# Optimization experiments

Hardware: AMD Instinct MI355X
Metric: run time of the kernel (lower is better)

## Reference

```python
import jax, jax.numpy as jnp
import numpy as np

MARGIN = 0.1
PD_EPS = 1e-6  # torch.nn.PairwiseDistance default eps (added to the difference)

B = 4096
D = 512


def setup_inputs() -> dict:
    key = jax.random.key(0)
    k1, k2, k3 = jax.random.split(key, 3)
    return {
        "feature_ts": jax.random.normal(k1, (B, D), dtype=jnp.float32),
        "feature_image1": jax.random.normal(k2, (B, D), dtype=jnp.float32),
        "feature_image2": jax.random.normal(k3, (B, D), dtype=jnp.float32),
    }


def _safe_sqrt(sq):
    # sqrt with zero gradient at 0 (matches torch.cdist backward at zero distance)
    pos = sq > 0
    return jnp.where(pos, jnp.sqrt(jnp.where(pos, sq, 1.0)), 0.0)


def reference(feature_ts, feature_image1, feature_image2):
    b, d = feature_ts.shape
    # representations: [3B, D]
    reps = jnp.concatenate([feature_ts, feature_image1, feature_image2], axis=0)

    # cdist(feature_ts, reps, p=2) -> [B, 3B] via Gram-matrix expansion
    sq = (
        jnp.sum(feature_ts * feature_ts, axis=1)[:, None]
        + jnp.sum(reps * reps, axis=1)[None, :]
        - 2.0 * (feature_ts @ reps.T)
    )
    dist = _safe_sqrt(jnp.maximum(sq, 0.0))          # [B, 3B]
    dist = jax.nn.relu(dist)                          # faithful (no-op: dist >= 0)

    # PairwiseDistance(p=2): ||x1 - x2 + eps||_2
    diff = feature_image1 - feature_image2 + PD_EPS
    dist12 = jnp.sqrt(jnp.sum(diff * diff, axis=1))   # [B]

    idx = jnp.arange(b)
    l_pos_1 = dist[idx, idx + b]                      # diag offset B
    l_pos_2 = dist[idx, idx + 2 * b]                  # diag offset 2B

    positives = l_pos_1 + l_pos_2 + dist12            # [B]
    positive_value = jnp.maximum(l_pos_1, l_pos_2)    # [B]

    # negatives: all columns except {i, i+B, i+2B}; masked min instead of gather
    cols = jnp.arange(3 * b)[None, :]
    rows = idx[:, None]
    same = (cols == rows) | (cols == rows + b) | (cols == rows + 2 * b)
    negative_value = jnp.min(jnp.where(same, jnp.inf, dist), axis=1)  # [B]

    triplet = jax.nn.relu(positives - negative_value + MARGIN) + positive_value
    return jnp.sum(triplet) / b
```

## Files before the change

### kernel.cpp

```cpp
#include <hip/hip_runtime.h>
#include <hip/hip_bf16.h>

typedef unsigned short u16;
typedef unsigned int u32;
typedef __attribute__((ext_vector_type(8))) short bf16x8;
typedef __attribute__((ext_vector_type(4))) float f32x4;

#define NB 4096
#define ND 512
#define NREPS (3*NB)
#define BM 128
#define BN 128
#define BK 64

#define GLD16(gp, lp)                                                         \
  __builtin_amdgcn_global_load_lds(                                           \
      (const __attribute__((address_space(1))) void*)(gp),                    \
      (__attribute__((address_space(3))) void*)(lp), 16, 0, 0)

__device__ __forceinline__ u16 f2bf(float f) {
  union { float f; u32 u; } v; v.f = f;
  u32 u = v.u;
  u32 r = (u + 0x7FFFu + ((u >> 16) & 1u)) >> 16;
  return (u16)r;
}

__global__ __launch_bounds__(256) void prep_all(
    const float* __restrict__ ts, const float* __restrict__ i1,
    const float* __restrict__ i2, u16* __restrict__ reps,
    float* __restrict__ norms, float* __restrict__ dist12,
    u32* __restrict__ minsq)
{
  __shared__ float s1[ND], s2[ND];
  const int r = blockIdx.x;
  const int tid = threadIdx.x;
  const int wave = tid >> 6, lane = tid & 63;

  if (wave < 3) {
    const float* src = (wave == 0) ? ts + (size_t)r * ND
                     : (wave == 1) ? i1 + (size_t)r * ND
                     :               i2 + (size_t)r * ND;
    const float4* s4 = (const float4*)src;
    float4 a = s4[lane*2+0];
    float4 b = s4[lane*2+1];
    if (wave == 1) { ((float4*)s1)[lane*2+0] = a; ((float4*)s1)[lane*2+1] = b; }
    if (wave == 2) { ((float4*)s2)[lane*2+0] = a; ((float4*)s2)[lane*2+1] = b; }
    float ss = a.x*a.x + a.y*a.y + a.z*a.z + a.w*a.w
             + b.x*b.x + b.y*b.y + b.z*b.z + b.w*b.w;
    uint4 pk;
    pk.x = (u32)f2bf(a.x) | ((u32)f2bf(a.y) << 16);
    pk.y = (u32)f2bf(a.z) | ((u32)f2bf(a.w) << 16);
    pk.z = (u32)f2bf(b.x) | ((u32)f2bf(b.y) << 16);
    pk.w = (u32)f2bf(b.z) | ((u32)f2bf(b.w) << 16);
    *(uint4*)(reps + (size_t)(wave*NB + r) * ND + lane*8) = pk;
    #pragma unroll
    for (int off = 32; off; off >>= 1) ss += __shfl_down(ss, off);
    if (lane == 0) norms[wave*NB + r] = ss;
  }
  __syncthreads();
  if (wave == 3) {
    float ss = 0.f;
    #pragma unroll
    for (int i = 0; i < 2; ++i) {
      float4 a = ((float4*)s1)[lane*2+i];
      float4 b = ((float4*)s2)[lane*2+i];
      float d0 = a.x - b.x + 1e-6f, d1 = a.y - b.y + 1e-6f;
      float d2 = a.z - b.z + 1e-6f, d3 = a.w - b.w + 1e-6f;
      ss += d0*d0 + d1*d1 + d2*d2 + d3*d3;
    }
    #pragma unroll
    for (int off = 32; off; off >>= 1) ss += __shfl_down(ss, off);
    if (lane == 0) { dist12[r] = sqrtf(ss); minsq[r] = 0x7F800000u; }
  }
}

__global__ __launch_bounds__(256) void gemm_min(
    const u16* __restrict__ reps, const float* __restrict__ norms,
    u32* __restrict__ minsq, float* __restrict__ lpos1,
    float* __restrict__ lpos2)
{
  __shared__ u16 As[BM*BK];
  __shared__ u16 Bs[BN*BK];
  const int tid  = threadIdx.x;
  const int lane = tid & 63;
  const int wave = tid >> 6;
  const int wr = wave >> 1, wc = wave & 1;
  const int fr = lane & 15, fg = lane >> 4;
  const int rowBase = blockIdx.x * BM;
  const int colBase = blockIdx.y * BN;

  const int rloc = lane >> 3;
  const int sp   = lane & 7;
  const u16* srcA[4]; const u16* srcB[4];
  u16* dstA[4]; u16* dstB[4];
  #pragma unroll
  for (int i = 0; i < 4; ++i) {
    const int r = wave*32 + i*8 + rloc;
    const int g = sp ^ (r & 7);
    srcA[i] = reps + (size_t)(rowBase + r) * ND + g*8;
    srcB[i] = reps + (size_t)(colBase + r) * ND + g*8;
    dstA[i] = &As[(wave*32 + i*8) * BK];
    dstB[i] = &Bs[(wave*32 + i*8) * BK];
  }

  f32x4 acc[4][4];
  const f32x4 zero = {0.f, 0.f, 0.f, 0.f};
  #pragma unroll
  for (int i = 0; i < 4; ++i)
    #pragma unroll
    for (int j = 0; j < 4; ++j)
      acc[i][j] = zero;

  for (int kt = 0; kt < ND/BK; ++kt) {
    const int koff = kt * BK;
    #pragma unroll
    for (int i = 0; i < 4; ++i) {
      GLD16(srcA[i] + koff, dstA[i]);
      GLD16(srcB[i] + koff, dstB[i]);
    }
    __syncthreads();

    bf16x8 af[4][2], bfrag[4][2];
    #pragma unroll
    for (int mf = 0; mf < 4; ++mf)
      #pragma unroll
      for (int ks = 0; ks < 2; ++ks) {
        const int rowA = wr*64 + mf*16 + fr;
        const int slot = ks*4 + fg;
        af[mf][ks]    = *(const bf16x8*)&As[rowA*BK + (slot ^ (rowA & 7))*8];
        const int rowB = wc*64 + mf*16 + fr;
        bfrag[mf][ks] = *(const bf16x8*)&Bs[rowB*BK + (slot ^ (rowB & 7))*8];
      }
    #pragma unroll
    for (int ks = 0; ks < 2; ++ks)
      #pragma unroll
      for (int mf = 0; mf < 4; ++mf)
        #pragma unroll
        for (int nf = 0; nf < 4; ++nf)
          acc[mf][nf] = __builtin_amdgcn_mfma_f32_16x16x32_bf16(
              af[mf][ks], bfrag[nf][ks], acc[mf][nf], 0, 0, 0);
    __syncthreads();
  }

  float ncol[4];
  #pragma unroll
  for (int nf = 0; nf < 4; ++nf)
    ncol[nf] = norms[colBase + wc*64 + nf*16 + fr];
  const float INF = __builtin_inff();
  #pragma unroll
  for (int mf = 0; mf < 4; ++mf) {
    #pragma unroll
    for (int q = 0; q < 4; ++q) {
      const int r_g = rowBase + wr*64 + mf*16 + fg*4 + q;
      const float ntr = norms[r_g];
      float vm = INF;
      #pragma unroll
      for (int nf = 0; nf < 4; ++nf) {
        const int c_g = colBase + wc*64 + nf*16 + fr;
        const float dot = acc[mf][nf][q];
        const float sq = ntr + ncol[nf] - 2.0f * dot;
        if (c_g == r_g + NB)   lpos1[r_g] = sq;
        if (c_g == r_g + 2*NB) lpos2[r_g] = sq;
        const bool excl = (c_g == r_g) || (c_g == r_g + NB) || (c_g == r_g + 2*NB);
        const float v = excl ? INF : fmaxf(sq, 0.0f);
        vm = fminf(vm, v);
      }
      #pragma unroll
      for (int off = 1; off < 16; off <<= 1)
        vm = fminf(vm, __shfl_xor(vm, off));
      if (fr == 0)
        atomicMin(minsq + r_g, __float_as_uint(vm));
    }
  }
}

__global__ __launch_bounds__(1024) void finalize(
    const float* __restrict__ lpos1, const float* __restrict__ lpos2,
    const float* __restrict__ dist12, const u32* __restrict__ minsq,
    float* __restrict__ out)
{
  __shared__ float red[16];
  const int tid = threadIdx.x;
  float s = 0.f;
  for (int r = tid; r < NB; r += 1024) {
    float l1 = sqrtf(fmaxf(lpos1[r], 0.f));
    float l2 = sqrtf(fmaxf(lpos2[r], 0.f));
    float neg = sqrtf(__uint_as_float(minsq[r]));
    float pos = l1 + l2 + dist12[r];
    s += fmaxf(pos - neg + 0.1f, 0.f) + fmaxf(l1, l2);
  }
  #pragma unroll
  for (int off = 32; off; off >>= 1) s += __shfl_down(s, off);
  if ((tid & 63) == 0) red[tid >> 6] = s;
  __syncthreads();
  if (tid == 0) {
    float t = 0.f;
    #pragma unroll
    for (int i = 0; i < 16; ++i) t += red[i];
    out[0] = t * (1.0f / NB);
  }
}

extern "C" void kernel_launch(void* const* d_in, const int* in_sizes, int n_in,
                              void* d_out, int out_size, void* d_ws, size_t ws_size,
                              hipStream_t stream) {
  const float* ts = (const float*)d_in[0];
  const float* i1 = (const float*)d_in[1];
  const float* i2 = (const float*)d_in[2];
  float* out = (float*)d_out;

  char* p = (char*)d_ws;
  u16* reps    = (u16*)p;            p += (size_t)NREPS * ND * sizeof(u16);
  float* norms = (float*)p;          p += (size_t)NREPS * sizeof(float);
  float* dist12 = (float*)p;         p += (size_t)NB * sizeof(float);
  u32* minsq   = (u32*)p;            p += (size_t)NB * sizeof(u32);
  float* lpos1 = (float*)p;          p += (size_t)NB * sizeof(float);
  float* lpos2 = (float*)p;          p += (size_t)NB * sizeof(float);

  prep_all<<<NB, 256, 0, stream>>>(ts, i1, i2, reps, norms, dist12, minsq);
  dim3 grid(NB / BM, NREPS / BN);
  gemm_min<<<grid, 256, 0, stream>>>(reps, norms, minsq, lpos1, lpos2);
  finalize<<<1, 1024, 0, stream>>>(lpos1, lpos2, dist12, minsq, out);
}
```

Before: 161.0 us.

## Use 256x256 tiles with double-buffered, quarter-staged load/MFMA pipeline

Grows the GEMM tile to 256x256 with 8 waves and double-buffers the LDS tiles. Global-to-LDS loads for the next k-step are split into quarters and interleaved with four MFMA quadrants, gated by explicit vmcnt waits, raw barriers and setprio. Workgroup IDs are remapped so neighbouring blocks share operand rows in L2. The aim is to hide load latency and raise data reuse per block, at the cost of more registers and LDS per block and a fragile hand-tuned wait schedule.

```diff
diff --git a/kernel.cpp b/kernel.cpp
--- a/kernel.cpp
+++ b/kernel.cpp
@@ -9,14 +9,18 @@
 #define NB 4096
 #define ND 512
 #define NREPS (3*NB)
-#define BM 128
-#define BN 128
+#define BM 256
+#define BN 256
 #define BK 64
+#define NKT (ND/BK)
+#define TSZ (BM*BK)
 
 #define GLD16(gp, lp)                                                         \
   __builtin_amdgcn_global_load_lds(                                           \
       (const __attribute__((address_space(1))) void*)(gp),                    \
       (__attribute__((address_space(3))) void*)(lp), 16, 0, 0)
+#define VMW asm volatile("s_waitcnt vmcnt(10)" ::: "memory")
+#define BAR __builtin_amdgcn_s_barrier()
 
 __device__ __forceinline__ u16 f2bf(float f) {
   union { float f; u32 u; } v; v.f = f;
@@ -74,72 +78,107 @@
   }
 }
 
-__global__ __launch_bounds__(256) void gemm_min(
+__device__ __forceinline__ void rdA(const u16* __restrict__ S, int wr, int fr,
+                                    int fg, int mfB, bf16x8 a[4][2]) {
+  #pragma unroll
+  for (int mf = 0; mf < 4; ++mf)
+    #pragma unroll
+    for (int ks = 0; ks < 2; ++ks) {
+      const int ra = wr*128 + (mfB+mf)*16 + fr;
+      a[mf][ks] = *(const bf16x8*)&S[ra*BK + ((ks*4+fg) ^ (ra & 7))*8];
+    }
+}
+__device__ __forceinline__ void rdB(const u16* __restrict__ S, int wc, int fr,
+                                    int fg, int nfB, bf16x8 b[2][2]) {
+  #pragma unroll
+  for (int nf = 0; nf < 2; ++nf)
+    #pragma unroll
+    for (int ks = 0; ks < 2; ++ks) {
+      const int rb = wc*64 + (nfB+nf)*16 + fr;
+      b[nf][ks] = *(const bf16x8*)&S[rb*BK + ((ks*4+fg) ^ (rb & 7))*8];
+    }
+}
+__device__ __forceinline__ void q_mfma(const bf16x8 a[4][2], const bf16x8 b[2][2],
+                                       f32x4 acc[8][4], int mfB, int nfB) {
+  #pragma unroll
+  for (int ks = 0; ks < 2; ++ks)
+    #pragma unroll
+    for (int mf = 0; mf < 4; ++mf)
+      #pragma unroll
+      for (int nf = 0; nf < 2; ++nf)
+        acc[mfB+mf][nfB+nf] = __builtin_amdgcn_mfma_f32_16x16x32_bf16(
+            a[mf][ks], b[nf][ks], acc[mfB+mf][nfB+nf], 0, 0, 0);
+}
+
+__global__ __launch_bounds__(512) void gemm_min(
     const u16* __restrict__ reps, const float* __restrict__ norms,
     u32* __restrict__ minsq, float* __restrict__ lpos1,
     float* __restrict__ lpos2)
 {
-  __shared__ u16 As[BM*BK];
-  __shared__ u16 Bs[BN*BK];
+  __shared__ u16 As[2*TSZ];
+  __shared__ u16 Bs[2*TSZ];
   const int tid  = threadIdx.x;
   const int lane = tid & 63;
   const int wave = tid >> 6;
-  const int wr = wave >> 1, wc = wave & 1;
+  const int wr = wave >> 2;
+  const int wc = wave & 3;
   const int fr = lane & 15, fg = lane >> 4;
-  const int rowBase = blockIdx.x * BM;
-  const int colBase = blockIdx.y * BN;
-
-  const int rloc = lane >> 3;
-  const int sp   = lane & 7;
-  const u16* srcA[4]; const u16* srcB[4];
-  u16* dstA[4]; u16* dstB[4];
-  #pragma unroll
-  for (int i = 0; i < 4; ++i) {
-    const int r = wave*32 + i*8 + rloc;
-    const int g = sp ^ (r & 7);
-    srcA[i] = reps + (size_t)(rowBase + r) * ND + g*8;
-    srcB[i] = reps + (size_t)(colBase + r) * ND + g*8;
-    dstA[i] = &As[(wave*32 + i*8) * BK];
-    dstB[i] = &Bs[(wave*32 + i*8) * BK];
-  }
-
-  f32x4 acc[4][4];
+
+  const int wid = (blockIdx.x & 7) * 96 + (blockIdx.x >> 3);
+  const int mx = wid & 15, ny = wid >> 4;
+  const int rowBase = mx * BM;
+  const int colBase = ny * BN;
+
+  const int c0 = wave * 2;
+  const int rA0 = (c0 < 8) ? c0*8 : 128 + (c0-8)*8;
+  const int rB0 = (c0 >> 2)*64 + (c0 & 3)*8;
+  const int gsw = (lane & 7) ^ (lane >> 3);
+  const u16* gA = reps + (size_t)(rowBase + rA0 + (lane>>3))*ND + gsw*8;
+  const u16* gB = reps + (size_t)(colBase + rB0 + (lane>>3))*ND + gsw*8;
+  u16* lA = As + rA0*BK;
+  u16* lB = Bs + rB0*BK;
+
+#define ST_ALO(b,k) { GLD16(gA + (k),         lA + (b)*TSZ);          \
+                      GLD16(gA + 8*ND + (k),  lA + (b)*TSZ + 8*BK); }
+#define ST_AHI(b,k) { GLD16(gA + 64*ND + (k), lA + (b)*TSZ + 64*BK);  \
+                      GLD16(gA + 72*ND + (k), lA + (b)*TSZ + 72*BK); }
+#define ST_BLO(b,k) { GLD16(gB + (k),         lB + (b)*TSZ);          \
+                      GLD16(gB + 8*ND + (k),  lB + (b)*TSZ + 8*BK); }
+#define ST_BHI(b,k) { GLD16(gB + 32*ND + (k), lB + (b)*TSZ + 32*BK);  \
+                      GLD16(gB + 40*ND + (k), lB + (b)*TSZ + 40*BK); }
+
+  f32x4 acc[8][4];
   const f32x4 zero = {0.f, 0.f, 0.f, 0.f};
   #pragma unroll
-  for (int i = 0; i < 4; ++i)
-    #pragma unroll
-    for (int j = 0; j < 4; ++j)
-      acc[i][j] = zero;
-
-  for (int kt = 0; kt < ND/BK; ++kt) {
-    const int koff = kt * BK;
-    #pragma unroll
-    for (int i = 0; i < 4; ++i) {
-      GLD16(srcA[i] + koff, dstA[i]);
-      GLD16(srcB[i] + koff, dstB[i]);
-    }
-    __syncthreads();
-
-    bf16x8 af[4][2], bfrag[4][2];
-    #pragma unroll
-    for (int mf = 0; mf < 4; ++mf)
-      #pragma unroll
-      for (int ks = 0; ks < 2; ++ks) {
-        const int rowA = wr*64 + mf*16 + fr;
-        const int slot = ks*4 + fg;
-        af[mf][ks]    = *(const bf16x8*)&As[rowA*BK + (slot ^ (rowA & 7))*8];
-        const int rowB = wc*64 + mf*16 + fr;
-        bfrag[mf][ks] = *(const bf16x8*)&Bs[rowB*BK + (slot ^ (rowB & 7))*8];
-      }
-    #pragma unroll
-    for (int ks = 0; ks < 2; ++ks)
-      #pragma unroll
-      for (int mf = 0; mf < 4; ++mf)
-        #pragma unroll
-        for (int nf = 0; nf < 4; ++nf)
-          acc[mf][nf] = __builtin_amdgcn_mfma_f32_16x16x32_bf16(
-              af[mf][ks], bfrag[nf][ks], acc[mf][nf], 0, 0, 0);
-    __syncthreads();
+  for (int i = 0; i < 8; ++i)
+    #pragma unroll
+    for (int j = 0; j < 4; ++j) acc[i][j] = zero;
+
+  bf16x8 aLo[4][2], aHi[4][2], bb[2][2];
+
+  ST_ALO(0, 0); ST_BLO(0, 0); ST_AHI(0, 0); ST_BHI(0, 0);
+  ST_ALO(1, BK); ST_BLO(1, BK); ST_AHI(1, BK);
+
+  for (int t = 0; t < NKT; ++t) {
+    const int cur = t & 1, nxt = cur ^ 1;
+    const u16* Sa = As + cur*TSZ;
+    const u16* Sb = Bs + cur*TSZ;
+    const int k1 = (t+1)*BK, k2 = (t+2)*BK;
+    VMW; ST_BHI(nxt, k1);
+    rdA(Sa, wr, fr, fg, 0, aLo); rdB(Sb, wc, fr, fg, 0, bb);
+    __builtin_amdgcn_s_setprio(1); q_mfma(aLo, bb, acc, 0, 0);
+    __builtin_amdgcn_s_setprio(0); BAR;
+    VMW; ST_ALO(cur, k2);
+    rdA(Sa, wr, fr, fg, 4, aHi);
+    __builtin_amdgcn_s_setprio(1); q_mfma(aHi, bb, acc, 4, 0);
+    __builtin_amdgcn_s_setprio(0); BAR;
+    VMW; ST_BLO(cur, k2);
+    rdB(Sb, wc, fr, fg, 2, bb);
+    __builtin_amdgcn_s_setprio(1); q_mfma(aLo, bb, acc, 0, 2);
+    __builtin_amdgcn_s_setprio(0); BAR;
+    VMW; ST_AHI(cur, k2);
+    __builtin_amdgcn_s_setprio(1); q_mfma(aHi, bb, acc, 4, 2);
+    __builtin_amdgcn_s_setprio(0); BAR;
   }
 
   float ncol[4];
@@ -148,10 +187,10 @@
     ncol[nf] = norms[colBase + wc*64 + nf*16 + fr];
   const float INF = __builtin_inff();
   #pragma unroll
-  for (int mf = 0; mf < 4; ++mf) {
+  for (int mf = 0; mf < 8; ++mf) {
     #pragma unroll
     for (int q = 0; q < 4; ++q) {
-      const int r_g = rowBase + wr*64 + mf*16 + fg*4 + q;
+      const int r_g = rowBase + wr*128 + mf*16 + fg*4 + q;
       const float ntr = norms[r_g];
       float vm = INF;
       #pragma unroll
@@ -218,7 +257,6 @@
   float* lpos2 = (float*)p;          p += (size_t)NB * sizeof(float);
 
   prep_all<<<NB, 256, 0, stream>>>(ts, i1, i2, reps, norms, dist12, minsq);
-  dim3 grid(NB / BM, NREPS / BN);
-  gemm_min<<<grid, 256, 0, stream>>>(reps, norms, minsq, lpos1, lpos2);
+  gemm_min<<<(NB/BM) * (NREPS/BN), 512, 0, stream>>>(reps, norms, minsq, lpos1, lpos2);
   finalize<<<1, 1024, 0, stream>>>(lpos1, lpos2, dist12, minsq, out);
 }
```

Result: slower. 189.2 us (+17.5%).

## Double-buffer LDS tiles in GEMM and remap blocks for XCD-aware locality

Applied to the files above, without the earlier changes.

Doubles the LDS A/B tiles so the global-to-LDS loads for the next K step are issued before the MFMA work on the current step, with one barrier per iteration instead of two. It also flattens the grid and remaps block IDs so consecutive blocks on each of the 8 XCDs cover nearby output tiles, aiming to improve L2 reuse. The cost is double the LDS per block (64KB), which may lower occupancy. The single barrier per iteration depends on the async LDS loads being complete by the time that barrier is reached.

```diff
diff --git a/kernel.cpp b/kernel.cpp
--- a/kernel.cpp
+++ b/kernel.cpp
@@ -12,6 +12,8 @@
 #define BM 128
 #define BN 128
 #define BK 64
+#define NKT (ND/BK)
+#define TSZ (BM*BK)
 
 #define GLD16(gp, lp)                                                         \
   __builtin_amdgcn_global_load_lds(                                           \
@@ -79,15 +81,19 @@
     u32* __restrict__ minsq, float* __restrict__ lpos1,
     float* __restrict__ lpos2)
 {
-  __shared__ u16 As[BM*BK];
-  __shared__ u16 Bs[BN*BK];
+  __shared__ u16 As[2*TSZ];
+  __shared__ u16 Bs[2*TSZ];
   const int tid  = threadIdx.x;
   const int lane = tid & 63;
   const int wave = tid >> 6;
   const int wr = wave >> 1, wc = wave & 1;
   const int fr = lane & 15, fg = lane >> 4;
-  const int rowBase = blockIdx.x * BM;
-  const int colBase = blockIdx.y * BN;
+
+  const int bid = blockIdx.x;
+  const int wid = (bid & 7) * 384 + (bid >> 3);
+  const int mx = wid / 96, ny = wid % 96;
+  const int rowBase = mx * BM;
+  const int colBase = ny * BN;
 
   const int rloc = lane >> 3;
   const int sp   = lane & 7;
@@ -103,6 +109,13 @@
     dstB[i] = &Bs[(wave*32 + i*8) * BK];
   }
 
+#define STAGE(buf, koff)                                                      \
+  { _Pragma("unroll")                                                         \
+    for (int i = 0; i < 4; ++i) {                                             \
+      GLD16(srcA[i] + (koff), dstA[i] + (buf)*TSZ);                           \
+      GLD16(srcB[i] + (koff), dstB[i] + (buf)*TSZ);                           \
+    } }
+
   f32x4 acc[4][4];
   const f32x4 zero = {0.f, 0.f, 0.f, 0.f};
   #pragma unroll
@@ -111,36 +124,39 @@
     for (int j = 0; j < 4; ++j)
       acc[i][j] = zero;
 
-  for (int kt = 0; kt < ND/BK; ++kt) {
-    const int koff = kt * BK;
-    #pragma unroll
-    for (int i = 0; i < 4; ++i) {
-      GLD16(srcA[i] + koff, dstA[i]);
-      GLD16(srcB[i] + koff, dstB[i]);
-    }
+#define COMPUTE(cur)                                                          \
+  { const u16* Sa = As + (cur)*TSZ;                                           \
+    const u16* Sb = Bs + (cur)*TSZ;                                           \
+    bf16x8 af[4][2], bfr[4][2];                                               \
+    _Pragma("unroll")                                                         \
+    for (int mf = 0; mf < 4; ++mf)                                            \
+      _Pragma("unroll")                                                       \
+      for (int ks = 0; ks < 2; ++ks) {                                        \
+        const int rowA = wr*64 + mf*16 + fr;                                  \
+        const int slot = ks*4 + fg;                                           \
+        af[mf][ks]  = *(const bf16x8*)&Sa[rowA*BK + (slot ^ (rowA & 7))*8];   \
+        const int rowB = wc*64 + mf*16 + fr;                                  \
+        bfr[mf][ks] = *(const bf16x8*)&Sb[rowB*BK + (slot ^ (rowB & 7))*8];   \
+      }                                                                       \
+    _Pragma("unroll")                                                         \
+    for (int ks = 0; ks < 2; ++ks)                                            \
+      _Pragma("unroll")                                                       \
+      for (int mf = 0; mf < 4; ++mf)                                          \
+        _Pragma("unroll")                                                     \
+        for (int nf = 0; nf < 4; ++nf)                                        \
+          acc[mf][nf] = __builtin_amdgcn_mfma_f32_16x16x32_bf16(              \
+              af[mf][ks], bfr[nf][ks], acc[mf][nf], 0, 0, 0);                 \
+  }
+
+  STAGE(0, 0);
+  __syncthreads();
+  #pragma unroll
+  for (int t = 0; t < NKT-1; ++t) {
+    STAGE((t & 1) ^ 1, (t+1)*BK);
+    COMPUTE(t & 1);
     __syncthreads();
-
-    bf16x8 af[4][2], bfrag[4][2];
-    #pragma unroll
-    for (int mf = 0; mf < 4; ++mf)
-      #pragma unroll
-      for (int ks = 0; ks < 2; ++ks) {
-        const int rowA = wr*64 + mf*16 + fr;
-        const int slot = ks*4 + fg;
-        af[mf][ks]    = *(const bf16x8*)&As[rowA*BK + (slot ^ (rowA & 7))*8];
-        const int rowB = wc*64 + mf*16 + fr;
-        bfrag[mf][ks] = *(const bf16x8*)&Bs[rowB*BK + (slot ^ (rowB & 7))*8];
-      }
-    #pragma unroll
-    for (int ks = 0; ks < 2; ++ks)
-      #pragma unroll
-      for (int mf = 0; mf < 4; ++mf)
-        #pragma unroll
-        for (int nf = 0; nf < 4; ++nf)
-          acc[mf][nf] = __builtin_amdgcn_mfma_f32_16x16x32_bf16(
-              af[mf][ks], bfrag[nf][ks], acc[mf][nf], 0, 0, 0);
-    __syncthreads();
-  }
+  }
+  COMPUTE((NKT-1) & 1);
 
   float ncol[4];
   #pragma unroll
@@ -218,7 +234,6 @@
   float* lpos2 = (float*)p;          p += (size_t)NB * sizeof(float);
 
   prep_all<<<NB, 256, 0, stream>>>(ts, i1, i2, reps, norms, dist12, minsq);
-  dim3 grid(NB / BM, NREPS / BN);
-  gemm_min<<<grid, 256, 0, stream>>>(reps, norms, minsq, lpos1, lpos2);
+  gemm_min<<<(NB/BM) * (NREPS/BN), 256, 0, stream>>>(reps, norms, minsq, lpos1, lpos2);
   finalize<<<1, 1024, 0, stream>>>(lpos1, lpos2, dist12, minsq, out);
 }
```

New measurement: 201.9 us. +25.4%, slower.
